# Optimization experiments

Hardware: AMD Instinct MI355X
Metric: run time of the kernel (lower is better)

## Reference

```python
import jax, jax.numpy as jnp
import numpy as np

H = 1024
V = 32000
L = 15
B = 512


def setup_inputs() -> dict:
    key = jax.random.key(0)
    ks = jax.random.split(key, 16)
    s = 0.02
    return {
        "input_ids": jax.random.randint(ks[0], (B,), 0, V),
        "hidden": jax.random.normal(ks[1], (1, B, H), jnp.float32),
        "encoder_outputs": jax.random.normal(ks[2], (L, B, H), jnp.float32),
        "max_length": L,
        "embedding": jax.random.normal(ks[3], (V, H), jnp.float32) * s,
        "attn1_w": jax.random.normal(ks[4], (1, 2 * H), jnp.float32) * s,
        "attn1_b": jnp.zeros((1,), jnp.float32),
        "combine_w": jax.random.normal(ks[5], (H, 2 * H), jnp.float32) * s,
        "combine_b": jnp.zeros((H,), jnp.float32),
        "w_ih": jax.random.normal(ks[6], (3 * H, H), jnp.float32) * s,
        "w_hh": jax.random.normal(ks[7], (3 * H, H), jnp.float32) * s,
        "b_ih": jnp.zeros((3 * H,), jnp.float32),
        "b_hh": jnp.zeros((3 * H,), jnp.float32),
        "out_w": jax.random.normal(ks[8], (V, H), jnp.float32) * s,
        "out_b": jnp.zeros((V,), jnp.float32),
    }


def reference(input_ids, hidden, encoder_outputs, max_length, embedding,
              attn1_w, attn1_b, combine_w, combine_b,
              w_ih, w_hh, b_ih, b_hh, out_w, out_b):
    # embedding lookup (dropout is identity in eval mode)
    emb = embedding[input_ids]                       # [B, H]
    # Bahdanau-style additive scores: vectorize the per-step python loop
    emb_l = jnp.broadcast_to(emb[None], (max_length, B, H))   # [L, B, H]
    cat = jnp.concatenate([emb_l, encoder_outputs], axis=-1)  # [L, B, 2H]
    scores = cat @ attn1_w.T + attn1_b               # [L, B, 1]
    attn_weights = jax.nn.softmax(scores, axis=0)    # softmax over L
    ctx = jnp.sum(attn_weights * encoder_outputs, axis=0)     # [B, H]
    x = jnp.concatenate([emb, ctx], axis=-1) @ combine_w.T + combine_b  # [B, H]
    # n_layers = 1: relu then one GRU step (seq len 1)
    x = jax.nn.relu(x)
    h = hidden[0]                                    # [B, H]
    gi = x @ w_ih.T + b_ih                           # [B, 3H]
    gh = h @ w_hh.T + b_hh                           # [B, 3H]
    i_r, i_z, i_n = jnp.split(gi, 3, axis=1)
    h_r, h_z, h_n = jnp.split(gh, 3, axis=1)
    r = jax.nn.sigmoid(i_r + h_r)
    z = jax.nn.sigmoid(i_z + h_z)
    n = jnp.tanh(i_n + r * h_n)
    h_new = (1.0 - z) * n + z * h                    # [B, H]
    logits = h_new @ out_w.T + out_b                 # [B, V]
    output = jax.nn.log_softmax(logits, axis=1)
    return output, h_new[None], attn_weights
```

## Files before the change

kernel.cpp:

```cpp
#include <hip/hip_runtime.h>

#define HH 1024
#define VV 32000
#define LL 15
#define BB 512

typedef __bf16 bf16;
typedef __bf16 bf16x4 __attribute__((ext_vector_type(4)));
typedef __bf16 bf16x8 __attribute__((ext_vector_type(8)));
typedef float f32x4 __attribute__((ext_vector_type(4)));

#define VMCNT(n) asm volatile("s_waitcnt vmcnt(" #n ")" ::: "memory")
#define SBAR     __builtin_amdgcn_s_barrier()
#define SCHED0   __builtin_amdgcn_sched_barrier(0)

__device__ __forceinline__ unsigned short f2bf(float f) {
    unsigned int u = __float_as_uint(f);
    unsigned int r = (u + 0x7fffu + ((u >> 16) & 1u)) >> 16;
    return (unsigned short)r;
}
__device__ __forceinline__ float bf2f(unsigned short u) {
    return __uint_as_float(((unsigned int)u) << 16);
}

__device__ __forceinline__ void gld_lds16(const void* g, void* l) {
    __builtin_amdgcn_global_load_lds(
        (const __attribute__((address_space(1))) unsigned int*)g,
        (__attribute__((address_space(3))) unsigned int*)l, 16, 0, 0);
}

#define NPACKB 2000
#define NCVTB  4352

__global__ __launch_bounds__(256)
void prologue(const float* __restrict__ out_w, unsigned short* __restrict__ packed,
              const float* __restrict__ w_ih, unsigned short* __restrict__ w_ih_bf,
              const float* __restrict__ w_hh, unsigned short* __restrict__ w_hh_bf,
              const float* __restrict__ combine_w, unsigned short* __restrict__ w_cb_bf,
              const float* __restrict__ hidden, unsigned short* __restrict__ hid_bf,
              const int* __restrict__ ids, const float* __restrict__ enc,
              const float* __restrict__ embedding,
              const float* __restrict__ attn1_w, const float* __restrict__ attn1_b,
              float* __restrict__ attn_out, unsigned short* __restrict__ cat_out) {
    __shared__ float s_enc[LL * HH];
    __shared__ float s_scores[LL];
    __shared__ float s_red[4];

    const int bid = blockIdx.x, tid = threadIdx.x;

    if (bid < NPACKB) {
        const int g = bid >> 3, rq = bid & 7;
        const float* s0 = out_w + ((size_t)g * 128 + rq * 16) * 1024;
        unsigned short* d0 = packed + (size_t)g * (16 * 128 * 64);
        #pragma unroll
        for (int j = 0; j < 16; j++) {
            const int s4 = j * 256 + tid;
            const f32x4 v = ((const f32x4*)s0)[s4];
            const int sp = s4 * 4;
            const int rl = rq * 16 + (sp >> 10);
            const int k = sp & 1023;
            bf16x4 w = __builtin_convertvector(v, bf16x4);
            *(bf16x4*)&d0[(size_t)(k >> 6) * 8192 + rl * 64 + (k & 63)] = w;
        }
        return;
    }
    if (bid < NPACKB + NCVTB) {
        int i = (bid - NPACKB) * 256 + tid;
        const float* src; unsigned short* dst;
        const int n0_ = 3 * HH * HH / 8, n1_ = 3 * HH * HH / 8;
        const int n2_ = 2 * HH * HH / 8, n3_ = BB * HH / 8;
        if (i < n0_) { src = w_ih; dst = w_ih_bf; }
        else if ((i -= n0_) < n1_) { src = w_hh; dst = w_hh_bf; }
        else if ((i -= n1_) < n2_) { src = combine_w; dst = w_cb_bf; }
        else if ((i -= n2_) < n3_) { src = hidden; dst = hid_bf; }
        else return;
        const f32x4 a = ((const f32x4*)src)[2 * i], b = ((const f32x4*)src)[2 * i + 1];
        ((bf16x4*)dst)[2 * i]     = __builtin_convertvector(a, bf16x4);
        ((bf16x4*)dst)[2 * i + 1] = __builtin_convertvector(b, bf16x4);
        return;
    }

    const int b = bid - (NPACKB + NCVTB);
    const int lane = tid & 63, wv = tid >> 6;

    for (int idx = tid; idx < LL * HH / 4; idx += 256) {
        const int l = (idx * 4) >> 10, h = (idx * 4) & (HH - 1);
        *(f32x4*)&s_enc[idx * 4] = *(const f32x4*)&enc[((size_t)l * BB + b) * HH + h];
    }

    const float* embr = embedding + (size_t)ids[b] * HH;
    float p = 0.f;
    for (int j = tid; j < HH; j += 256) p += embr[j] * attn1_w[j];
    #pragma unroll
    for (int o = 32; o; o >>= 1) p += __shfl_xor(p, o);
    if (lane == 0) s_red[wv] = p;
    __syncthreads();
    const float semb = s_red[0] + s_red[1] + s_red[2] + s_red[3] + attn1_b[0];

    for (int l = wv; l < LL; l += 4) {
        float q = 0.f;
        for (int j = lane; j < HH; j += 64) q += s_enc[l * HH + j] * attn1_w[HH + j];
        #pragma unroll
        for (int o = 32; o; o >>= 1) q += __shfl_xor(q, o);
        if (lane == 0) s_scores[l] = q + semb;
    }
    __syncthreads();

    float mx = -3.4e38f;
    #pragma unroll
    for (int l = 0; l < LL; l++) mx = fmaxf(mx, s_scores[l]);
    float aw[LL], sum = 0.f;
    #pragma unroll
    for (int l = 0; l < LL; l++) { aw[l] = __expf(s_scores[l] - mx); sum += aw[l]; }
    const float inv = 1.f / sum;
    #pragma unroll
    for (int l = 0; l < LL; l++) aw[l] *= inv;

    if (tid < LL) attn_out[tid * BB + b] = aw[tid];

    for (int j = tid; j < HH; j += 256) {
        float c = 0.f;
        #pragma unroll
        for (int l = 0; l < LL; l++) c += aw[l] * s_enc[l * HH + j];
        cat_out[(size_t)b * (2 * HH) + j] = f2bf(embr[j]);
        cat_out[(size_t)b * (2 * HH) + HH + j] = f2bf(c);
    }
}

template<int TM, int TN, int OUT, int GATES>
__global__ __launch_bounds__(256)
void gemm_nt(const bf16* __restrict__ A, const bf16* __restrict__ B,
             const float* __restrict__ bias, void* __restrict__ Cout,
             const bf16* __restrict__ A2, const bf16* __restrict__ B2,
             const float* __restrict__ bias2, void* __restrict__ C2,
             const int K, const int N) {
    constexpr int FM = TM / 32, FN = TN / 32;
    __shared__ bf16 As[2][TM * 64];
    __shared__ bf16 Bs[2][TN * 64];

    if (GATES && blockIdx.z == 1) { A = A2; B = B2; bias = bias2; Cout = C2; }

    const int tid = threadIdx.x;
    const int lane = tid & 63, wave = tid >> 6;
    const int wm = wave >> 1, wn = wave & 1;
    const int rlo = lane & 15, khi = lane >> 4;
    const int m0 = blockIdx.y * TM, n0 = blockIdx.x * TN;

    f32x4 acc[FM][FN] = {};
    constexpr int IA = TM / 32, IB = TN / 32;

    auto stage = [&](int k0, int buf) {
        #pragma unroll
        for (int i = 0; i < IA; i++) {
            const int p = (i * 256 + tid) * 16;
            const int row = p >> 7;
            const int qs = (p & 127) ^ ((row & 7) << 4);
            gld_lds16(A + (size_t)(m0 + row) * K + k0 + (qs >> 1),
                      &As[buf][0] + i * 2048 + wave * 512);
        }
        #pragma unroll
        for (int i = 0; i < IB; i++) {
            const int p = (i * 256 + tid) * 16;
            const int row = p >> 7;
            const int qs = (p & 127) ^ ((row & 7) << 4);
            gld_lds16(B + (size_t)(n0 + row) * K + k0 + (qs >> 1),
                      &Bs[buf][0] + i * 2048 + wave * 512);
        }
    };

    auto compute = [&](int buf) {
        #pragma unroll
        for (int ks = 0; ks < 2; ks++) {
            bf16x8 af[FM], bfr[FN];
            #pragma unroll
            for (int m = 0; m < FM; m++) {
                const int r = wm * (TM / 2) + m * 16 + rlo;
                const int sw = (ks * 64 + khi * 16) ^ ((r & 7) << 4);
                af[m] = *(const bf16x8*)((const char*)&As[buf][0] + r * 128 + sw);
            }
            #pragma unroll
            for (int n = 0; n < FN; n++) {
                const int r = wn * (TN / 2) + n * 16 + rlo;
                const int sw = (ks * 64 + khi * 16) ^ ((r & 7) << 4);
                bfr[n] = *(const bf16x8*)((const char*)&Bs[buf][0] + r * 128 + sw);
            }
            #pragma unroll
            for (int m = 0; m < FM; m++)
                #pragma unroll
                for (int n = 0; n < FN; n++)
                    acc[m][n] = __builtin_amdgcn_mfma_f32_16x16x32_bf16(af[m], bfr[n], acc[m][n], 0, 0, 0);
        }
    };

    const int NT = K >> 6;
    stage(0, 0);
    stage(64, 1);

    for (int kt = 0; kt < NT; kt += 2) {
        {
            const int t = kt;
            if (t + 1 < NT) { VMCNT(4); } else { VMCNT(0); }
            SCHED0; SBAR; SCHED0;
            compute(0);
            SCHED0; SBAR; SCHED0;
            if (t + 2 < NT) stage((t + 2) << 6, 0);
        }
        {
            const int t = kt + 1;
            if (t + 1 < NT) { VMCNT(4); } else { VMCNT(0); }
            SCHED0; SBAR; SCHED0;
            compute(1);
            SCHED0; SBAR; SCHED0;
            if (t + 2 < NT) stage((t + 2) << 6, 1);
        }
    }

    #pragma unroll
    for (int m = 0; m < FM; m++) {
        const int gr = m0 + wm * (TM / 2) + m * 16 + khi * 4;
        #pragma unroll
        for (int n = 0; n < FN; n++) {
            const int gc = n0 + wn * (TN / 2) + n * 16 + rlo;
            const float bv = bias[gc];
            #pragma unroll
            for (int j = 0; j < 4; j++) {
                float v = acc[m][n][j] + bv;
                if (OUT == 1) {
                    v = fmaxf(v, 0.f);
                    ((unsigned short*)Cout)[(size_t)(gr + j) * N + gc] = f2bf(v);
                } else {
                    ((float*)Cout)[(size_t)(gr + j) * N + gc] = v;
                }
            }
        }
    }
}

template<int CB>
__global__ __launch_bounds__(256, 2)
void gemm_out(const bf16* __restrict__ A, const bf16* __restrict__ Bp,
              const float* __restrict__ bias, float* __restrict__ C,
              unsigned short* __restrict__ Cb,
              float* __restrict__ pmax, float* __restrict__ psum) {
    constexpr int K = HH, N = VV;
    __shared__ bf16 As[2][128 * 64];
    __shared__ bf16 Bs[2][128 * 64];
    __shared__ float sPm[2][128], sPs[2][128];

    const int tid = threadIdx.x;
    const int lane = tid & 63, wave = tid >> 6;
    const int wm = wave >> 1, wn = wave & 1;
    const int rlo = lane & 15, khi = lane >> 4;

    constexpr int gridN = 250;
    constexpr int nFull = (gridN >> 3) << 5;
    const int bidx = blockIdx.x;
    int g, jm;
    if (bidx < nFull) { const int s = bidx >> 5, rem = bidx & 31; jm = rem >> 3; g = s * 8 + (rem & 7); }
    else { const int rem = bidx - nFull; constexpr int gleft = gridN & 7; g = (gridN & ~7) + rem % gleft; jm = rem / gleft; }
    const int n0 = g * 128, m0 = jm * 128;

    const char* pb = (const char*)(Bp + (size_t)g * 131072);

    f32x4 acc[4][4] = {};

    auto stage = [&](int k0, int buf) {
        #pragma unroll
        for (int i = 0; i < 4; i++) {
            const int p = (i * 256 + tid) * 16;
            const int row = p >> 7;
            const int qs = (p & 127) ^ ((row & 7) << 4);
            gld_lds16(A + (size_t)(m0 + row) * K + k0 + (qs >> 1),
                      &As[buf][0] + i * 2048 + wave * 512);
        }
        #pragma unroll
        for (int i = 0; i < 4; i++) {
            const int p = (i * 256 + tid) * 16;
            const int row = p >> 7;
            const int qs = (p & 127) ^ ((row & 7) << 4);
            gld_lds16(pb + (size_t)(k0 >> 6) * 16384 + row * 128 + qs,
                      &Bs[buf][0] + i * 2048 + wave * 512);
        }
    };

    auto compute = [&](int buf) {
        #pragma unroll
        for (int ks = 0; ks < 2; ks++) {
            bf16x8 af[4], bfr[4];
            #pragma unroll
            for (int m = 0; m < 4; m++) {
                const int r = wm * 64 + m * 16 + rlo;
                const int sw = (ks * 64 + khi * 16) ^ ((r & 7) << 4);
                af[m] = *(const bf16x8*)((const char*)&As[buf][0] + r * 128 + sw);
            }
            #pragma unroll
            for (int n = 0; n < 4; n++) {
                const int r = wn * 64 + n * 16 + rlo;
                const int sw = (ks * 64 + khi * 16) ^ ((r & 7) << 4);
                bfr[n] = *(const bf16x8*)((const char*)&Bs[buf][0] + r * 128 + sw);
            }
            #pragma unroll
            for (int m = 0; m < 4; m++)
                #pragma unroll
                for (int n = 0; n < 4; n++)
                    acc[m][n] = __builtin_amdgcn_mfma_f32_16x16x32_bf16(af[m], bfr[n], acc[m][n], 0, 0, 0);
        }
    };

    constexpr int NT = K >> 6;
    stage(0, 0);
    stage(64, 1);

    for (int kt = 0; kt < NT; kt += 2) {
        {
            const int t = kt;
            if (t + 1 < NT) { VMCNT(8); } else { VMCNT(0); }
            SCHED0; SBAR; SCHED0;
            compute(0);
            SCHED0; SBAR; SCHED0;
            if (t + 2 < NT) stage((t + 2) << 6, 0);
        }
        {
            const int t = kt + 1;
            if (t + 1 < NT) { VMCNT(8); } else { VMCNT(0); }
            SCHED0; SBAR; SCHED0;
            compute(1);
            SCHED0; SBAR; SCHED0;
            if (t + 2 < NT) stage((t + 2) << 6, 1);
        }
    }

    float bvn[4];
    #pragma unroll
    for (int n = 0; n < 4; n++) bvn[n] = bias[n0 + wn * 64 + n * 16 + rlo];

    #pragma unroll
    for (int m = 0; m < 4; m++) {
        const int rbase = wm * 64 + m * 16 + khi * 4;
        #pragma unroll
        for (int j = 0; j < 4; j++) {
            const int gr = m0 + rbase + j;
            float v[4];
            float lm = -3.4e38f;
            #pragma unroll
            for (int n = 0; n < 4; n++) {
                v[n] = acc[m][n][j] + bvn[n];
                const size_t ci = (size_t)gr * N + n0 + wn * 64 + n * 16 + rlo;
                if (CB) Cb[ci] = f2bf(v[n]); else C[ci] = v[n];
                lm = fmaxf(lm, v[n]);
            }
            #pragma unroll
            for (int o = 8; o; o >>= 1) lm = fmaxf(lm, __shfl_xor(lm, o));
            float ls = 0.f;
            #pragma unroll
            for (int n = 0; n < 4; n++) ls += __expf(v[n] - lm);
            #pragma unroll
            for (int o = 8; o; o >>= 1) ls += __shfl_xor(ls, o);
            if (rlo == 0) { sPm[wn][rbase + j] = lm; sPs[wn][rbase + j] = ls; }
        }
    }
    __syncthreads();
    if (tid < 128) {
        const float ma = sPm[0][tid], mb = sPm[1][tid];
        const float M = fmaxf(ma, mb);
        const float S = sPs[0][tid] * __expf(ma - M) + sPs[1][tid] * __expf(mb - M);
        pmax[(size_t)(m0 + tid) * 256 + g] = M;
        psum[(size_t)(m0 + tid) * 256 + g] = S;
    }
}

__global__ __launch_bounds__(256)
void gru_kernel(const float* __restrict__ gi, const float* __restrict__ gh,
                const float* __restrict__ h, float* __restrict__ hnew,
                unsigned short* __restrict__ hnew_bf) {
    const int i = blockIdx.x * 256 + threadIdx.x;
    const int e = i * 4;
    const int b = e >> 10, j = e & (HH - 1);
    const size_t o = ((size_t)b * 3 * HH + j) / 4;
    const f32x4 ir = ((const f32x4*)gi)[o],          iz = ((const f32x4*)gi)[o + HH / 4],
                in_ = ((const f32x4*)gi)[o + 2 * HH / 4];
    const f32x4 hr = ((const f32x4*)gh)[o],          hz = ((const f32x4*)gh)[o + HH / 4],
                hn = ((const f32x4*)gh)[o + 2 * HH / 4];
    const f32x4 hv = ((const f32x4*)h)[i];
    f32x4 out;
    ushort4 ob;
    #pragma unroll
    for (int c = 0; c < 4; c++) {
        const float r = 1.f / (1.f + __expf(-(ir[c] + hr[c])));
        const float z = 1.f / (1.f + __expf(-(iz[c] + hz[c])));
        const float n = tanhf(in_[c] + r * hn[c]);
        const float v = (1.f - z) * n + z * hv[c];
        out[c] = v;
        ((unsigned short*)&ob)[c] = f2bf(v);
    }
    ((f32x4*)hnew)[i] = out;
    ((ushort4*)hnew_bf)[i] = ob;
}

template<int CB>
__global__ __launch_bounds__(512)
void lsm_final(const float* __restrict__ pmax, const float* __restrict__ psum,
               const unsigned short* __restrict__ Cb, float* __restrict__ logits) {
    const int b = blockIdx.x, tid = threadIdx.x;
    const int lane = tid & 63, wv = tid >> 6;
    __shared__ float sm[8], ss[8];

    float m = -3.4e38f, s = 0.f;
    if (tid < 250) { m = pmax[(size_t)b * 256 + tid]; s = psum[(size_t)b * 256 + tid]; }
    #pragma unroll
    for (int o = 32; o; o >>= 1) {
        const float mo = __shfl_xor(m, o), so = __shfl_xor(s, o);
        const float nm = fmaxf(m, mo);
        s = s * __expf(m - nm) + so * __expf(mo - nm);
        m = nm;
    }
    if (lane == 0) { sm[wv] = m; ss[wv] = s; }
    __syncthreads();
    float M = sm[0], S;
    #pragma unroll
    for (int w = 1; w < 8; w++) M = fmaxf(M, sm[w]);
    S = ss[0] * __expf(sm[0] - M);
    #pragma unroll
    for (int w = 1; w < 8; w++) S += ss[w] * __expf(sm[w] - M);
    const float lse = M + __logf(S);

    float* row = logits + (size_t)b * VV;
    if (CB) {
        const unsigned short* rowc = Cb + (size_t)b * VV;
        for (int j = tid; j < VV / 8; j += 512) {
            const ushort4 u0 = ((const ushort4*)rowc)[2 * j];
            const ushort4 u1 = ((const ushort4*)rowc)[2 * j + 1];
            f32x4 v0, v1;
            v0[0] = bf2f(u0.x) - lse; v0[1] = bf2f(u0.y) - lse;
            v0[2] = bf2f(u0.z) - lse; v0[3] = bf2f(u0.w) - lse;
            v1[0] = bf2f(u1.x) - lse; v1[1] = bf2f(u1.y) - lse;
            v1[2] = bf2f(u1.z) - lse; v1[3] = bf2f(u1.w) - lse;
            ((f32x4*)row)[2 * j] = v0;
            ((f32x4*)row)[2 * j + 1] = v1;
        }
    } else {
        for (int j = tid; j < VV / 4; j += 512) {
            f32x4 v = ((const f32x4*)row)[j];
            v[0] -= lse; v[1] -= lse; v[2] -= lse; v[3] -= lse;
            ((f32x4*)row)[j] = v;
        }
    }
}

extern "C" void kernel_launch(void* const* d_in, const int* in_sizes, int n_in,
                              void* d_out, int out_size, void* d_ws, size_t ws_size,
                              hipStream_t stream) {
    const int*   ids       = (const int*)d_in[0];
    const float* hidden    = (const float*)d_in[1];
    const float* enc       = (const float*)d_in[2];
    const float* embedding = (const float*)d_in[4];
    const float* attn1_w   = (const float*)d_in[5];
    const float* attn1_b   = (const float*)d_in[6];
    const float* combine_w = (const float*)d_in[7];
    const float* combine_b = (const float*)d_in[8];
    const float* w_ih      = (const float*)d_in[9];
    const float* w_hh      = (const float*)d_in[10];
    const float* b_ih      = (const float*)d_in[11];
    const float* b_hh      = (const float*)d_in[12];
    const float* out_w     = (const float*)d_in[13];
    const float* out_b     = (const float*)d_in[14];

    float* out_lsm = (float*)d_out;
    float* out_h   = out_lsm + (size_t)BB * VV;
    float* out_aw  = out_h + (size_t)BB * HH;

    char* w = (char*)d_ws;
    unsigned short* packed   = (unsigned short*)w;   w += (size_t)VV * HH * 2;
    unsigned short* w_ih_bf  = (unsigned short*)w;   w += (size_t)3 * HH * HH * 2;
    unsigned short* w_hh_bf  = (unsigned short*)w;   w += (size_t)3 * HH * HH * 2;
    unsigned short* w_cb_bf  = (unsigned short*)w;   w += (size_t)2 * HH * HH * 2;
    unsigned short* cat_bf   = (unsigned short*)w;   w += (size_t)BB * 2 * HH * 2;
    unsigned short* x_bf     = (unsigned short*)w;   w += (size_t)BB * HH * 2;
    unsigned short* hid_bf   = (unsigned short*)w;   w += (size_t)BB * HH * 2;
    unsigned short* hnew_bf  = (unsigned short*)w;   w += (size_t)BB * HH * 2;
    float* gi   = (float*)w;                         w += (size_t)BB * 3 * HH * 4;
    float* gh   = (float*)w;                         w += (size_t)BB * 3 * HH * 4;
    float* pmax = (float*)w;                         w += (size_t)BB * 256 * 4;
    float* psum = (float*)w;                         w += (size_t)BB * 256 * 4;
    unsigned short* Cb = (unsigned short*)w;
    const size_t needed_cb = (size_t)(w - (char*)d_ws) + (size_t)BB * VV * 2;
    const bool use_cb = ws_size >= needed_cb;

    prologue<<<NPACKB + NCVTB + BB, 256, 0, stream>>>(
        out_w, packed, w_ih, w_ih_bf, w_hh, w_hh_bf, combine_w, w_cb_bf,
        hidden, hid_bf, ids, enc, embedding, attn1_w, attn1_b, out_aw, cat_bf);

    gemm_nt<64, 64, 1, 0><<<dim3(HH / 64, BB / 64), 256, 0, stream>>>(
        (const bf16*)cat_bf, (const bf16*)w_cb_bf, combine_b, x_bf,
        nullptr, nullptr, nullptr, nullptr, 2 * HH, HH);

    gemm_nt<64, 64, 0, 1><<<dim3(3 * HH / 64, BB / 64, 2), 256, 0, stream>>>(
        (const bf16*)hid_bf, (const bf16*)w_hh_bf, b_hh, gh,
        (const bf16*)x_bf, (const bf16*)w_ih_bf, b_ih, gi, HH, 3 * HH);

    gru_kernel<<<(BB * HH / 4) / 256, 256, 0, stream>>>(gi, gh, hidden, out_h, hnew_bf);

    if (use_cb) {
        gemm_out<1><<<1000, 256, 0, stream>>>(
            (const bf16*)hnew_bf, (const bf16*)packed, out_b, nullptr, Cb, pmax, psum);
        lsm_final<1><<<BB, 512, 0, stream>>>(pmax, psum, Cb, out_lsm);
    } else {
        gemm_out<0><<<1000, 256, 0, stream>>>(
            (const bf16*)hnew_bf, (const bf16*)packed, out_b, out_lsm, nullptr, pmax, psum);
        lsm_final<0><<<BB, 512, 0, stream>>>(pmax, psum, nullptr, out_lsm);
    }
}
```

Measured before the change: 171.9 us.

## Reorder prologue blocks, coarsen conversion work, stage out_w packing through LDS

The prologue now schedules the long-running attention blocks first, so they no longer form a tail at the end of the launch. Each weight-conversion block now handles four chunks, cutting the block count by four. The out_w packing now stages a 64x512 tile as bf16 in LDS and writes 16-byte contiguous chunks to the packed layout instead of scattered 8-byte stores. The cost is a 64KB LDS allocation shared by all block types, which may lower occupancy, and fewer blocks for the packing work.

```diff
diff --git a/kernel.cpp b/kernel.cpp
--- a/kernel.cpp
+++ b/kernel.cpp
@@ -29,8 +29,9 @@
         (__attribute__((address_space(3))) unsigned int*)l, 16, 0, 0);
 }
 
-#define NPACKB 2000
-#define NCVTB  4352
+#define NATT  512
+#define NCVT  1088
+#define NPACK 1000
 
 __global__ __launch_bounds__(256)
 void prologue(const float* __restrict__ out_w, unsigned short* __restrict__ packed,
@@ -42,88 +43,109 @@
               const float* __restrict__ embedding,
               const float* __restrict__ attn1_w, const float* __restrict__ attn1_b,
               float* __restrict__ attn_out, unsigned short* __restrict__ cat_out) {
-    __shared__ float s_enc[LL * HH];
+    __shared__ __align__(16) char smem[65536];
     __shared__ float s_scores[LL];
     __shared__ float s_red[4];
 
     const int bid = blockIdx.x, tid = threadIdx.x;
 
-    if (bid < NPACKB) {
-        const int g = bid >> 3, rq = bid & 7;
-        const float* s0 = out_w + ((size_t)g * 128 + rq * 16) * 1024;
-        unsigned short* d0 = packed + (size_t)g * (16 * 128 * 64);
-        #pragma unroll
-        for (int j = 0; j < 16; j++) {
-            const int s4 = j * 256 + tid;
-            const f32x4 v = ((const f32x4*)s0)[s4];
-            const int sp = s4 * 4;
-            const int rl = rq * 16 + (sp >> 10);
-            const int k = sp & 1023;
-            bf16x4 w = __builtin_convertvector(v, bf16x4);
-            *(bf16x4*)&d0[(size_t)(k >> 6) * 8192 + rl * 64 + (k & 63)] = w;
+    if (bid < NATT) {
+        const int b = bid;
+        const int lane = tid & 63, wv = tid >> 6;
+        float* s_enc = (float*)smem;
+
+        for (int idx = tid; idx < LL * HH / 4; idx += 256) {
+            const int l = (idx * 4) >> 10, h = (idx * 4) & (HH - 1);
+            *(f32x4*)&s_enc[idx * 4] = *(const f32x4*)&enc[((size_t)l * BB + b) * HH + h];
+        }
+
+        const float* embr = embedding + (size_t)ids[b] * HH;
+        float p = 0.f;
+        for (int j = tid; j < HH; j += 256) p += embr[j] * attn1_w[j];
+        #pragma unroll
+        for (int o = 32; o; o >>= 1) p += __shfl_xor(p, o);
+        if (lane == 0) s_red[wv] = p;
+        __syncthreads();
+        const float semb = s_red[0] + s_red[1] + s_red[2] + s_red[3] + attn1_b[0];
+
+        for (int l = wv; l < LL; l += 4) {
+            float q = 0.f;
+            for (int j = lane; j < HH; j += 64) q += s_enc[l * HH + j] * attn1_w[HH + j];
+            #pragma unroll
+            for (int o = 32; o; o >>= 1) q += __shfl_xor(q, o);
+            if (lane == 0) s_scores[l] = q + semb;
+        }
+        __syncthreads();
+
+        float mx = -3.4e38f;
+        #pragma unroll
+        for (int l = 0; l < LL; l++) mx = fmaxf(mx, s_scores[l]);
+        float aw[LL], sum = 0.f;
+        #pragma unroll
+        for (int l = 0; l < LL; l++) { aw[l] = __expf(s_scores[l] - mx); sum += aw[l]; }
+        const float inv = 1.f / sum;
+        #pragma unroll
+        for (int l = 0; l < LL; l++) aw[l] *= inv;
+
+        if (tid < LL) attn_out[tid * BB + b] = aw[tid];
+
+        for (int j = tid; j < HH; j += 256) {
+            float c = 0.f;
+            #pragma unroll
+            for (int l = 0; l < LL; l++) c += aw[l] * s_enc[l * HH + j];
+            cat_out[(size_t)b * (2 * HH) + j] = f2bf(embr[j]);
+            cat_out[(size_t)b * (2 * HH) + HH + j] = f2bf(c);
         }
         return;
     }
-    if (bid < NPACKB + NCVTB) {
-        int i = (bid - NPACKB) * 256 + tid;
-        const float* src; unsigned short* dst;
+
+    if (bid < NATT + NCVT) {
+        const int base = (bid - NATT) * 1024 + tid;
         const int n0_ = 3 * HH * HH / 8, n1_ = 3 * HH * HH / 8;
         const int n2_ = 2 * HH * HH / 8, n3_ = BB * HH / 8;
-        if (i < n0_) { src = w_ih; dst = w_ih_bf; }
-        else if ((i -= n0_) < n1_) { src = w_hh; dst = w_hh_bf; }
-        else if ((i -= n1_) < n2_) { src = combine_w; dst = w_cb_bf; }
-        else if ((i -= n2_) < n3_) { src = hidden; dst = hid_bf; }
-        else return;
-        const f32x4 a = ((const f32x4*)src)[2 * i], b = ((const f32x4*)src)[2 * i + 1];
-        ((bf16x4*)dst)[2 * i]     = __builtin_convertvector(a, bf16x4);
-        ((bf16x4*)dst)[2 * i + 1] = __builtin_convertvector(b, bf16x4);
+        #pragma unroll
+        for (int q = 0; q < 4; q++) {
+            int i = base + q * 256;
+            const float* src; unsigned short* dst;
+            if (i < n0_) { src = w_ih; dst = w_ih_bf; }
+            else if ((i -= n0_) < n1_) { src = w_hh; dst = w_hh_bf; }
+            else if ((i -= n1_) < n2_) { src = combine_w; dst = w_cb_bf; }
+            else if ((i -= n2_) < n3_) { src = hidden; dst = hid_bf; }
+            else continue;
+            const f32x4 a = ((const f32x4*)src)[2 * i], b = ((const f32x4*)src)[2 * i + 1];
+            ((bf16x4*)dst)[2 * i]     = __builtin_convertvector(a, bf16x4);
+            ((bf16x4*)dst)[2 * i + 1] = __builtin_convertvector(b, bf16x4);
+        }
         return;
     }
 
-    const int b = bid - (NPACKB + NCVTB);
-    const int lane = tid & 63, wv = tid >> 6;
-
-    for (int idx = tid; idx < LL * HH / 4; idx += 256) {
-        const int l = (idx * 4) >> 10, h = (idx * 4) & (HH - 1);
-        *(f32x4*)&s_enc[idx * 4] = *(const f32x4*)&enc[((size_t)l * BB + b) * HH + h];
-    }
-
-    const float* embr = embedding + (size_t)ids[b] * HH;
-    float p = 0.f;
-    for (int j = tid; j < HH; j += 256) p += embr[j] * attn1_w[j];
-    #pragma unroll
-    for (int o = 32; o; o >>= 1) p += __shfl_xor(p, o);
-    if (lane == 0) s_red[wv] = p;
+    const int bid2 = bid - (NATT + NCVT);
+    const int rg = bid2 >> 1;
+    const int ks = bid2 & 1;
+    const int g  = rg >> 1;
+    const int half = rg & 1;
+    unsigned short* sm = (unsigned short*)smem;
+
+    const float* src = out_w + (size_t)(rg * 64) * 1024 + ks * 512;
+    #pragma unroll
+    for (int it = 0; it < 32; ++it) {
+        const int u = it * 256 + tid;
+        const int r = u >> 7, c4 = u & 127;
+        const f32x4 v = *(const f32x4*)(src + (size_t)r * 1024 + c4 * 4);
+        const bf16x4 w = __builtin_convertvector(v, bf16x4);
+        *(bf16x4*)&sm[r * 512 + c4 * 4] = w;
+    }
     __syncthreads();
-    const float semb = s_red[0] + s_red[1] + s_red[2] + s_red[3] + attn1_b[0];
-
-    for (int l = wv; l < LL; l += 4) {
-        float q = 0.f;
-        for (int j = lane; j < HH; j += 64) q += s_enc[l * HH + j] * attn1_w[HH + j];
-        #pragma unroll
-        for (int o = 32; o; o >>= 1) q += __shfl_xor(q, o);
-        if (lane == 0) s_scores[l] = q + semb;
-    }
-    __syncthreads();
-
-    float mx = -3.4e38f;
-    #pragma unroll
-    for (int l = 0; l < LL; l++) mx = fmaxf(mx, s_scores[l]);
-    float aw[LL], sum = 0.f;
-    #pragma unroll
-    for (int l = 0; l < LL; l++) { aw[l] = __expf(s_scores[l] - mx); sum += aw[l]; }
-    const float inv = 1.f / sum;
-    #pragma unroll
-    for (int l = 0; l < LL; l++) aw[l] *= inv;
-
-    if (tid < LL) attn_out[tid * BB + b] = aw[tid];
-
-    for (int j = tid; j < HH; j += 256) {
-        float c = 0.f;
-        #pragma unroll
-        for (int l = 0; l < LL; l++) c += aw[l] * s_enc[l * HH + j];
-        cat_out[(size_t)b * (2 * HH) + j] = f2bf(embr[j]);
-        cat_out[(size_t)b * (2 * HH) + HH + j] = f2bf(c);
+
+    char* dst = (char*)packed + (size_t)g * 262144 + (size_t)half * 8192;
+    #pragma unroll
+    for (int it = 0; it < 16; ++it) {
+        const int v16 = it * 256 + tid;
+        const int ktl = v16 >> 9;
+        const int o   = v16 & 511;
+        const int rr  = o >> 3, oc = o & 7;
+        const bf16x8 val = *(const bf16x8*)&sm[rr * 512 + ktl * 64 + oc * 8];
+        *(bf16x8*)(dst + (size_t)(ks * 8 + ktl) * 16384 + rr * 128 + oc * 16) = val;
     }
 }
 
@@ -486,7 +508,7 @@
     const size_t needed_cb = (size_t)(w - (char*)d_ws) + (size_t)BB * VV * 2;
     const bool use_cb = ws_size >= needed_cb;
 
-    prologue<<<NPACKB + NCVTB + BB, 256, 0, stream>>>(
+    prologue<<<NATT + NCVT + NPACK, 256, 0, stream>>>(
         out_w, packed, w_ih, w_ih_bf, w_hh, w_hh_bf, combine_w, w_cb_bf,
         hidden, hid_bf, ids, enc, embedding, attn1_w, attn1_b, out_aw, cat_bf);
 
```

Result: slower. 179.9 us (+4.6%).
